# Optimization experiments

Hardware: AMD Instinct MI355X
Metric: run time of the kernel (lower is better)

The kernel has to match this reference:

```python
import jax, jax.numpy as jnp
import numpy as np

D_MODEL = 1024
D_K = 1024
B, T = 4, 2048


def setup_inputs() -> dict:
    key = jax.random.key(0)
    kx, kq, kk, kv = jax.random.split(key, 4)
    s = 1.0 / np.sqrt(D_MODEL)
    return {
        "x": jax.random.normal(kx, (B, T, D_MODEL), dtype=jnp.float32),
        "W_q": jax.random.normal(kq, (D_MODEL, D_K), dtype=jnp.float32) * s,
        "W_k": jax.random.normal(kk, (D_MODEL, D_K), dtype=jnp.float32) * s,
        "W_v": jax.random.normal(kv, (D_MODEL, D_K), dtype=jnp.float32) * s,
    }


def reference(x, W_q, W_k, W_v):
    # x: (B, T, C); W_*: (C, d_k). Linear(no bias) == x @ W
    q = jnp.einsum('btc,ck->btk', x, W_q)
    k = jnp.einsum('btc,ck->btk', x, W_k)
    v = jnp.einsum('btc,ck->btk', x, W_v)
    d_k = W_q.shape[1]
    scores = jnp.einsum('bqk,bsk->bqs', q, k) / jnp.sqrt(jnp.asarray(d_k, x.dtype))
    T_ = x.shape[1]
    causal = jnp.tril(jnp.ones((T_, T_), dtype=bool))
    scores = jnp.where(causal, scores, jnp.asarray(-jnp.inf, scores.dtype))
    weights = jax.nn.softmax(scores, axis=-1)
    return jnp.einsum('bqs,bsk->bqk', weights, v)
```

## Files before the change

### kernel.cpp

```cpp
#include <hip/hip_runtime.h>
#include <hip/hip_bf16.h>
#include <stdint.h>

typedef __bf16 bf16x8 __attribute__((ext_vector_type(8)));
typedef float  f32x4  __attribute__((ext_vector_type(4)));
typedef unsigned int u32x4 __attribute__((ext_vector_type(4)));

__device__ __forceinline__ unsigned short f2bf(float x) {
    union { float f; unsigned u; } v; v.f = x;
    unsigned r = v.u + 0x7fffu + ((v.u >> 16) & 1u);
    return (unsigned short)(r >> 16);
}

__device__ __forceinline__ float bf2f(unsigned short b) {
    union { unsigned u; float f; } v; v.u = ((unsigned)b) << 16; return v.f;
}

__device__ __forceinline__ void async16(const void* g, void* l) {
    __builtin_amdgcn_global_load_lds(
        (const __attribute__((address_space(1))) void*)g,
        (__attribute__((address_space(3))) void*)l,
        16, 0, 0);
}

template <typename OutT, bool CAUSAL_SKIP, bool KLIMIT, bool VFOLD>
__global__ __launch_bounds__(256, 3) void gemm_bt(
    const unsigned short* __restrict__ A,
    const unsigned short* __restrict__ Bt,
    OutT* __restrict__ C,
    unsigned short* __restrict__ VtOut,
    int M, int N, int K, int lda, int ldb, int ldc,
    int ldvt, int nsplit,
    long long sA, long long sB, long long sC, long long sVt, float scale)
{
    const int bn = blockIdx.x, bz = blockIdx.z;
    const int bm = KLIMIT ? (gridDim.y - 1 - blockIdx.y) : blockIdx.y;
    if (CAUSAL_SKIP && bn > bm) return;

    A  += (long long)bz * sA;
    Bt += (long long)bz * sB;
    C  += (long long)bz * sC;

    const int m0 = bm * 128, n0 = bn * 128;
    const int Keff = KLIMIT ? min(K, (bm + 1) * 128) : K;

    __shared__ __align__(16) unsigned short LDS[2 * 2 * 128 * 32];

    const int tid  = threadIdx.x;
    const int w    = tid >> 6, l = tid & 63;
    const int wr   = w >> 1,  wc = w & 1;
    const int lrow = l & 15,  quad = l >> 4;

    f32x4 acc[4][4] = {};

    const int rA0  = 32 * w + (l >> 2);
    const int cOff = (((l & 3) ^ ((l >> 3) & 3))) * 8;
    const unsigned short* aG0 = A  + (long long)(m0 + rA0)      * lda + cOff;
    const unsigned short* aG1 = A  + (long long)(m0 + rA0 + 16) * lda + cOff;
    const unsigned short* bG0 = Bt + (long long)(n0 + rA0)      * ldb + cOff;
    const unsigned short* bG1 = Bt + (long long)(n0 + rA0 + 16) * ldb + cOff;
    unsigned short* aL = &LDS[(2 * w) * 512 + l * 8];
    unsigned short* bL = aL + 4096;

    const int sl = (lrow >> 1) & 3;

    async16(aG0, aL);
    async16(aG1, aL + 512);
    async16(bG0, bL);
    async16(bG1, bL + 512);

    for (int k0 = 0; k0 < Keff; k0 += 32) {
        const int cur = ((k0 >> 5) & 1) * 8192;
        __syncthreads();

        if (k0 + 32 < Keff) {
            const int nxt = cur ^ 8192;
            async16(aG0 + k0 + 32, aL + nxt);
            async16(aG1 + k0 + 32, aL + nxt + 512);
            async16(bG0 + k0 + 32, bL + nxt);
            async16(bG1 + k0 + 32, bL + nxt + 512);
        }

        const unsigned short* As = &LDS[cur];
        const unsigned short* Bs = &LDS[cur + 4096];
        bf16x8 af[4], bfr[4];
#pragma unroll
        for (int i = 0; i < 4; i++) {
            af[i]  = *(const bf16x8*)&As[(wr * 64 + i * 16 + lrow) * 32 + (quad ^ sl) * 8];
            bfr[i] = *(const bf16x8*)&Bs[(wc * 64 + i * 16 + lrow) * 32 + (quad ^ sl) * 8];
        }
#pragma unroll
        for (int i = 0; i < 4; i++)
#pragma unroll
            for (int j = 0; j < 4; j++)
                acc[i][j] = __builtin_amdgcn_mfma_f32_16x16x32_bf16(af[i], bfr[j], acc[i][j], 0, 0, 0);
    }

    if constexpr (VFOLD) {
        if (n0 >= nsplit) {
            unsigned short* Vp = VtOut + (long long)bz * sVt;
#pragma unroll
            for (int i = 0; i < 4; i++) {
                const int t = m0 + wr * 64 + i * 16 + quad * 4;
#pragma unroll
                for (int j = 0; j < 4; j++) {
                    const int d = (n0 - nsplit) + wc * 64 + j * 16 + lrow;
                    union { unsigned short u[4]; uint2 p; } o;
#pragma unroll
                    for (int r = 0; r < 4; r++) o.u[r] = f2bf(acc[i][j][r] * scale);
                    *(uint2*)(Vp + (long long)d * ldvt + t) = o.p;
                }
            }
            return;
        }
    }

    __syncthreads();

    char* eb = (char*)LDS + w * 2288;
    const int erow = l >> 2, ep = l & 3;

    if constexpr (sizeof(OutT) == 2) {
#pragma unroll
        for (int i = 0; i < 4; i++) {
#pragma unroll
            for (int j = 0; j < 4; j++)
#pragma unroll
                for (int r = 0; r < 4; r++)
                    *(unsigned short*)(eb + (quad * 4 + r) * 144 + (j * 16 + lrow) * 2) =
                        f2bf(acc[i][j][r] * scale);
            const long long gm = m0 + wr * 64 + i * 16 + erow;
#pragma unroll
            for (int c = 0; c < 2; c++) {
                u32x4 d = *(u32x4*)(eb + erow * 144 + ep * 32 + c * 16);
                *(u32x4*)((unsigned short*)C + gm * ldc + (n0 + wc * 64 + ep * 16 + c * 8)) = d;
            }
        }
    } else {
#pragma unroll
        for (int i = 0; i < 4; i++) {
            const long long gm = m0 + wr * 64 + i * 16 + erow;
#pragma unroll
            for (int jc = 0; jc < 2; jc++) {
#pragma unroll
                for (int jj = 0; jj < 2; jj++)
#pragma unroll
                    for (int r = 0; r < 4; r++)
                        *(float*)(eb + (quad * 4 + r) * 144 + (jj * 16 + lrow) * 4) =
                            acc[i][2 * jc + jj][r] * scale;
#pragma unroll
                for (int c = 0; c < 2; c++) {
                    f32x4 d = *(f32x4*)(eb + erow * 144 + ep * 32 + c * 16);
                    *(f32x4*)((float*)C + gm * ldc + (n0 + wc * 64 + jc * 32 + ep * 8 + c * 4)) = d;
                }
            }
        }
    }
}

__global__ __launch_bounds__(256) void cast_f32_bf16(
    const float4* __restrict__ in, unsigned short* __restrict__ out, int n4)
{
    int i = blockIdx.x * 256 + threadIdx.x;
    if (i >= n4) return;
    float4 v = in[i];
    union { unsigned short u[4]; uint2 p; } o;
    o.u[0] = f2bf(v.x); o.u[1] = f2bf(v.y); o.u[2] = f2bf(v.z); o.u[3] = f2bf(v.w);
    *(uint2*)(out + (long long)i * 4) = o.p;
}

__global__ __launch_bounds__(256) void transpose_cast_w3(
    const float* __restrict__ W0, const float* __restrict__ W1,
    const float* __restrict__ W2, unsigned short* __restrict__ out, int n)
{
    const float* in = (blockIdx.z == 0) ? W0 : (blockIdx.z == 1) ? W1 : W2;
    out += (long long)blockIdx.z * n * n;
    __shared__ float tile[32][33];
    const int tx = threadIdx.x, ty = threadIdx.y;
    const int c0 = blockIdx.x * 32, r0 = blockIdx.y * 32;
#pragma unroll
    for (int i = 0; i < 4; i++)
        tile[ty + i * 8][tx] = in[(long long)(r0 + ty + i * 8) * n + c0 + tx];
    __syncthreads();
#pragma unroll
    for (int i = 0; i < 4; i++)
        out[(long long)(c0 + ty + i * 8) * n + r0 + tx] = f2bf(tile[tx][ty + i * 8]);
}

__global__ __launch_bounds__(256) void causal_softmax_bf16(
    const unsigned short* __restrict__ S, unsigned short* __restrict__ P, int T)
{
    const int row = blockIdx.x;
    const int t   = row & (T - 1);
    const int L   = t + 1;
    const unsigned short* s = S + (long long)row * T;
    unsigned short* p = P + (long long)row * T;
    const int tid  = threadIdx.x;
    const int base = tid * 8;

    uint4 raw = *(const uint4*)(s + base);
    unsigned rr[4] = {raw.x, raw.y, raw.z, raw.w};
    float v[8];
#pragma unroll
    for (int k = 0; k < 4; k++) {
        union { unsigned u; float f; } a, b;
        a.u = (rr[k] & 0xFFFFu) << 16;
        b.u = rr[k] & 0xFFFF0000u;
        v[2 * k] = a.f; v[2 * k + 1] = b.f;
    }
    float mx = -3.0e38f;
#pragma unroll
    for (int k = 0; k < 8; k++) {
        if (base + k >= L) v[k] = -3.0e38f;
        mx = fmaxf(mx, v[k]);
    }
#pragma unroll
    for (int off = 32; off; off >>= 1) mx = fmaxf(mx, __shfl_xor(mx, off));
    __shared__ float red[4], red2[4];
    const int wid = tid >> 6, lid = tid & 63;
    if (lid == 0) red[wid] = mx;
    __syncthreads();
    mx = fmaxf(fmaxf(red[0], red[1]), fmaxf(red[2], red[3]));

    float sum = 0.f;
#pragma unroll
    for (int k = 0; k < 8; k++) { v[k] = __expf(v[k] - mx); sum += v[k]; }
#pragma unroll
    for (int off = 32; off; off >>= 1) sum += __shfl_xor(sum, off);
    if (lid == 0) red2[wid] = sum;
    __syncthreads();
    sum = red2[0] + red2[1] + red2[2] + red2[3];
    const float inv = 1.0f / sum;

    union { unsigned short u[8]; uint4 q; } o;
#pragma unroll
    for (int k = 0; k < 8; k++) o.u[k] = f2bf(v[k] * inv);
    *(uint4*)(p + base) = o.q;
}

extern "C" void kernel_launch(void* const* d_in, const int* in_sizes, int n_in,
                              void* d_out, int out_size, void* d_ws, size_t ws_size,
                              hipStream_t stream)
{
    const int B = 4, T = 2048, C = 1024, D = 1024;
    const float* x  = (const float*)d_in[0];
    const float* Wq = (const float*)d_in[1];
    const float* Wk = (const float*)d_in[2];
    const float* Wv = (const float*)d_in[3];
    float* out = (float*)d_out;
    char* ws = (char*)d_ws;

    const size_t MB = 1ull << 20;
    unsigned short* Xbf   = (unsigned short*)(ws + 0);
    unsigned short* WqkvT = (unsigned short*)(ws + 16 * MB);
    unsigned short* QK    = (unsigned short*)(ws + 22 * MB);
    unsigned short* Vt    = (unsigned short*)(ws + 54 * MB);
    unsigned short* Sbf   = (unsigned short*)(ws + 70 * MB);
    unsigned short* P     = (unsigned short*)(ws + 0);

    const long long sX  = (long long)T * C;
    const long long sQK = (long long)T * 2 * D;
    const long long sVt = (long long)D * T;
    const long long sS  = (long long)T * T;
    const long long sO  = (long long)T * D;

    {
        int n4 = B * T * C / 4;
        cast_f32_bf16<<<dim3((n4 + 255) / 256), dim3(256), 0, stream>>>(
            (const float4*)x, Xbf, n4);
    }
    {
        dim3 g(32, 32, 3), b(32, 8);
        transpose_cast_w3<<<g, b, 0, stream>>>(Wq, Wk, Wv, WqkvT, 1024);
    }
    {
        dim3 g(3072 / 128, 2048 / 128, 4), b(256);
        gemm_bt<unsigned short, false, false, true><<<g, b, 0, stream>>>(
            Xbf, WqkvT, QK, Vt, 2048, 3072, 1024, 1024, 1024, 2048,
             T,  2048, sX, 0, sQK, sVt, 1.0f);
    }
    {
        dim3 g(2048 / 128, 2048 / 128, 4), b(256);
        gemm_bt<unsigned short, true, false, false><<<g, b, 0, stream>>>(
            QK, QK + D, Sbf, nullptr, 2048, 2048, 1024, 2 * D, 2 * D, 2048,
            0, 0, sQK, sQK, sS, 0, 0.03125f);
    }
    {
        causal_softmax_bf16<<<dim3(B * T), dim3(256), 0, stream>>>(Sbf, P, T);
    }
    {
        dim3 g(1024 / 128, 2048 / 128, 4), b(256);
        gemm_bt<float, false, true, false><<<g, b, 0, stream>>>(
            P, Vt, out, nullptr, 2048, 1024, 2048, 2048, 2048, 1024,
            0, 0, sS, sVt, sO, 0, 1.0f);
    }
    (void)in_sizes; (void)n_in; (void)out_size; (void)ws_size;
}
```

Before: 251.7 us.

## Split-K the causal PV GEMM for long row tiles and merge partials

Row tiles 8-15 of the P·V GEMM are split at K=1024 into two blocks, each writing a float partial, and a new merge kernel sums them into the output. Rows 0-7 still write directly. This evens out the causal triangle's per-tile work so the longest blocks no longer dominate the tail. The cost is 32 MB of extra float partial traffic and one extra launch. The softmax also stops loading S entries beyond the causal length.

```diff
diff --git a/kernel.cpp b/kernel.cpp
--- a/kernel.cpp
+++ b/kernel.cpp
@@ -10,10 +10,6 @@
     union { float f; unsigned u; } v; v.f = x;
     unsigned r = v.u + 0x7fffu + ((v.u >> 16) & 1u);
     return (unsigned short)(r >> 16);
-}
-
-__device__ __forceinline__ float bf2f(unsigned short b) {
-    union { unsigned u; float f; } v; v.u = ((unsigned)b) << 16; return v.f;
 }
 
 __device__ __forceinline__ void async16(const void* g, void* l) {
@@ -23,18 +19,30 @@
         16, 0, 0);
 }
 
-template <typename OutT, bool CAUSAL_SKIP, bool KLIMIT, bool VFOLD>
+template <typename OutT, bool CAUSAL_SKIP, bool VFOLD, bool SPLITK>
 __global__ __launch_bounds__(256, 3) void gemm_bt(
     const unsigned short* __restrict__ A,
     const unsigned short* __restrict__ Bt,
     OutT* __restrict__ C,
     unsigned short* __restrict__ VtOut,
+    float* __restrict__ Part0,
+    float* __restrict__ Part1,
     int M, int N, int K, int lda, int ldb, int ldc,
     int ldvt, int nsplit,
-    long long sA, long long sB, long long sC, long long sVt, float scale)
+    long long sA, long long sB, long long sC, long long sVt, long long sPart,
+    float scale)
 {
     const int bn = blockIdx.x, bz = blockIdx.z;
-    const int bm = KLIMIT ? (gridDim.y - 1 - blockIdx.y) : blockIdx.y;
+
+    int bm, kbeg, kend;
+    bool part = false;
+    if constexpr (SPLITK) {
+        const int y = blockIdx.y;
+        if (y < 8) { bm = 15 - y; part = true;  kbeg = 1024; kend = (bm + 1) * 128; }
+        else       { bm = 23 - y; part = false; kbeg = 0;    kend = min(1024, (bm + 1) * 128); }
+    } else {
+        bm = blockIdx.y; kbeg = 0; kend = K;
+    }
     if (CAUSAL_SKIP && bn > bm) return;
 
     A  += (long long)bz * sA;
@@ -42,7 +50,6 @@
     C  += (long long)bz * sC;
 
     const int m0 = bm * 128, n0 = bn * 128;
-    const int Keff = KLIMIT ? min(K, (bm + 1) * 128) : K;
 
     __shared__ __align__(16) unsigned short LDS[2 * 2 * 128 * 32];
 
@@ -64,16 +71,16 @@
 
     const int sl = (lrow >> 1) & 3;
 
-    async16(aG0, aL);
-    async16(aG1, aL + 512);
-    async16(bG0, bL);
-    async16(bG1, bL + 512);
-
-    for (int k0 = 0; k0 < Keff; k0 += 32) {
+    async16(aG0 + kbeg, aL);
+    async16(aG1 + kbeg, aL + 512);
+    async16(bG0 + kbeg, bL);
+    async16(bG1 + kbeg, bL + 512);
+
+    for (int k0 = kbeg; k0 < kend; k0 += 32) {
         const int cur = ((k0 >> 5) & 1) * 8192;
         __syncthreads();
 
-        if (k0 + 32 < Keff) {
+        if (k0 + 32 < kend) {
             const int nxt = cur ^ 8192;
             async16(aG0 + k0 + 32, aL + nxt);
             async16(aG1 + k0 + 32, aL + nxt + 512);
@@ -137,6 +144,14 @@
             }
         }
     } else {
+        float* fbase;
+        if constexpr (SPLITK) {
+            if (part)            fbase = Part1 + (long long)bz * sPart - (long long)1024 * ldc;
+            else if (bm >= 8)    fbase = Part0 + (long long)bz * sPart - (long long)1024 * ldc;
+            else                 fbase = (float*)C;
+        } else {
+            fbase = (float*)C;
+        }
 #pragma unroll
         for (int i = 0; i < 4; i++) {
             const long long gm = m0 + wr * 64 + i * 16 + erow;
@@ -151,11 +166,24 @@
 #pragma unroll
                 for (int c = 0; c < 2; c++) {
                     f32x4 d = *(f32x4*)(eb + erow * 144 + ep * 32 + c * 16);
-                    *(f32x4*)((float*)C + gm * ldc + (n0 + wc * 64 + jc * 32 + ep * 8 + c * 4)) = d;
+                    *(f32x4*)(fbase + gm * ldc + (n0 + wc * 64 + jc * 32 + ep * 8 + c * 4)) = d;
                 }
             }
         }
     }
+}
+
+__global__ __launch_bounds__(256) void merge_part(
+    float* __restrict__ out, const float* __restrict__ p0, const float* __restrict__ p1)
+{
+    const int i = blockIdx.x * 256 + threadIdx.x;
+    const int bz = i >> 18;
+    const int r  = i & 262143;
+    const float4* a4 = (const float4*)(p0 + (long long)bz * 1048576) + r;
+    const float4* b4 = (const float4*)(p1 + (long long)bz * 1048576) + r;
+    float4 a = *a4, b = *b4;
+    a.x += b.x; a.y += b.y; a.z += b.z; a.w += b.w;
+    *((float4*)(out + (long long)bz * 2097152 + 1048576) + r) = a;
 }
 
 __global__ __launch_bounds__(256) void cast_f32_bf16(
@@ -198,7 +226,7 @@
     const int tid  = threadIdx.x;
     const int base = tid * 8;
 
-    uint4 raw = *(const uint4*)(s + base);
+    uint4 raw = (base < L) ? *(const uint4*)(s + base) : make_uint4(0, 0, 0, 0);
     unsigned rr[4] = {raw.x, raw.y, raw.z, raw.w};
     float v[8];
 #pragma unroll
@@ -251,18 +279,21 @@
     char* ws = (char*)d_ws;
 
     const size_t MB = 1ull << 20;
-    unsigned short* Xbf   = (unsigned short*)(ws + 0);
-    unsigned short* WqkvT = (unsigned short*)(ws + 16 * MB);
-    unsigned short* QK    = (unsigned short*)(ws + 22 * MB);
-    unsigned short* Vt    = (unsigned short*)(ws + 54 * MB);
-    unsigned short* Sbf   = (unsigned short*)(ws + 70 * MB);
-    unsigned short* P     = (unsigned short*)(ws + 0);
+    unsigned short* Xbf    = (unsigned short*)(ws + 0);
+    unsigned short* WqkvT  = (unsigned short*)(ws + 16 * MB);
+    unsigned short* QK     = (unsigned short*)(ws + 22 * MB);
+    unsigned short* Vt     = (unsigned short*)(ws + 54 * MB);
+    unsigned short* Sbf    = (unsigned short*)(ws + 70 * MB);
+    float*          Opart1 = (float*)(ws + 102 * MB);
+    float*          Opart0 = (float*)(ws + 118 * MB);
+    unsigned short* P      = (unsigned short*)(ws + 0);
 
     const long long sX  = (long long)T * C;
     const long long sQK = (long long)T * 2 * D;
     const long long sVt = (long long)D * T;
     const long long sS  = (long long)T * T;
     const long long sO  = (long long)T * D;
+    const long long sP2 = (long long)1024 * 1024;
 
     {
         int n4 = B * T * C / 4;
@@ -275,24 +306,27 @@
     }
     {
         dim3 g(3072 / 128, 2048 / 128, 4), b(256);
-        gemm_bt<unsigned short, false, false, true><<<g, b, 0, stream>>>(
-            Xbf, WqkvT, QK, Vt, 2048, 3072, 1024, 1024, 1024, 2048,
-             T,  2048, sX, 0, sQK, sVt, 1.0f);
+        gemm_bt<unsigned short, false, true, false><<<g, b, 0, stream>>>(
+            Xbf, WqkvT, QK, Vt, nullptr, nullptr, 2048, 3072, 1024, 1024, 1024, 2048,
+             T,  2048, sX, 0, sQK, sVt, 0, 1.0f);
     }
     {
         dim3 g(2048 / 128, 2048 / 128, 4), b(256);
         gemm_bt<unsigned short, true, false, false><<<g, b, 0, stream>>>(
-            QK, QK + D, Sbf, nullptr, 2048, 2048, 1024, 2 * D, 2 * D, 2048,
-            0, 0, sQK, sQK, sS, 0, 0.03125f);
+            QK, QK + D, Sbf, nullptr, nullptr, nullptr, 2048, 2048, 1024, 2 * D, 2 * D, 2048,
+            0, 0, sQK, sQK, sS, 0, 0, 0.03125f);
     }
     {
         causal_softmax_bf16<<<dim3(B * T), dim3(256), 0, stream>>>(Sbf, P, T);
     }
     {
-        dim3 g(1024 / 128, 2048 / 128, 4), b(256);
-        gemm_bt<float, false, true, false><<<g, b, 0, stream>>>(
-            P, Vt, out, nullptr, 2048, 1024, 2048, 2048, 2048, 1024,
-            0, 0, sS, sVt, sO, 0, 1.0f);
+        dim3 g(1024 / 128, 24, 4), b(256);
+        gemm_bt<float, false, false, true><<<g, b, 0, stream>>>(
+            P, Vt, out, nullptr, Opart0, Opart1, 2048, 1024, 2048, 2048, 2048, 1024,
+            0, 0, sS, sVt, sO, 0, sP2, 1.0f);
+    }
+    {
+        merge_part<<<dim3(4096), dim3(256), 0, stream>>>(out, Opart0, Opart1);
     }
     (void)in_sizes; (void)n_in; (void)out_size; (void)ws_size;
 }
```

After: 253.0 us. No clear change (+0.5%).
